# Kernel optimization log

Measured on AMD Instinct MI355X. Metric: run time of the kernel, lower is better.

Reference implementation:

```python
import jax, jax.numpy as jnp
import numpy as np

N_P, N_D, N_S = 100000, 1000, 5000      # patients, drugs, diseases
C, H, L = 64, 4, 2                       # hidden, heads, layers
DH = C // H                              # head dim
IN_P, IN_D, IN_S = 64, 128, 64           # raw feature dims per node type
E_PD, E_DP, E_DS, E_PS = 300000, 300000, 100000, 100000
EPS = 1e-16


def setup_inputs() -> dict:
    key = jax.random.key(0)
    ks = jax.random.split(key, 20)

    def lin(k, fin, fout, prefix=()):
        return jax.random.normal(k, prefix + (fin, fout), jnp.float32) / np.sqrt(fin).astype(np.float32)

    def edges(k, e, n_src, n_dst):
        k1, k2 = jax.random.split(k)
        return jnp.stack([jax.random.randint(k1, (e,), 0, n_src),
                          jax.random.randint(k2, (e,), 0, n_dst)]).astype(jnp.int32)

    inp = {}
    inp['x_p'] = jax.random.normal(ks[0], (N_P, IN_P), jnp.float32)
    inp['x_d'] = jax.random.normal(ks[1], (N_D, IN_D), jnp.float32)
    inp['x_s'] = jax.random.normal(ks[2], (N_S, IN_S), jnp.float32)
    inp['Win_p'] = lin(ks[3], IN_P, C); inp['bin_p'] = jnp.zeros((C,), jnp.float32)
    inp['Win_d'] = lin(ks[4], IN_D, C); inp['bin_d'] = jnp.zeros((C,), jnp.float32)
    inp['Win_s'] = lin(ks[5], IN_S, C); inp['bin_s'] = jnp.zeros((C,), jnp.float32)
    inp['Wk'] = lin(ks[6], C, C, (L, 3)); inp['bk'] = jnp.zeros((L, 3, C), jnp.float32)
    inp['Wq'] = lin(ks[7], C, C, (L, 3)); inp['bq'] = jnp.zeros((L, 3, C), jnp.float32)
    inp['Wv'] = lin(ks[8], C, C, (L, 3)); inp['bv'] = jnp.zeros((L, 3, C), jnp.float32)
    inp['Wa'] = lin(ks[9], C, C, (L, 3)); inp['ba'] = jnp.zeros((L, 3, C), jnp.float32)
    inp['a_rel'] = jax.random.normal(ks[10], (L, 4, H, DH, DH), jnp.float32) / np.sqrt(DH).astype(np.float32)
    inp['m_rel'] = jax.random.normal(ks[11], (L, 4, H, DH, DH), jnp.float32) / np.sqrt(DH).astype(np.float32)
    inp['p_rel'] = jnp.ones((L, 4, H), jnp.float32)   # PyG inits rel prior to ones
    inp['skip'] = jnp.ones((L, 3), jnp.float32)       # PyG inits skip gate to ones
    inp['ei_pd'] = edges(ks[12], E_PD, N_P, N_D)  # patient -takes-> drug
    inp['ei_dp'] = edges(ks[13], E_DP, N_D, N_P)  # drug -taken_by-> patient
    inp['ei_ds'] = edges(ks[14], E_DS, N_D, N_S)  # drug -treats-> disease
    inp['ei_ps'] = edges(ks[15], E_PS, N_P, N_S)  # patient -has-> disease
    return inp


def _hgt(x_p, x_d, x_s, Win_p, bin_p, Win_d, bin_d, Win_s, bin_s,
         Wk, bk, Wq, bq, Wv, bv, Wa, ba, a_rel, m_rel, p_rel, skip,
         ei_pd, ei_dp, ei_ds, ei_ps):
    Ns = (N_P, N_D, N_S)
    # per-node-type input projection (lin_dict)
    xs = [x_p @ Win_p + bin_p, x_d @ Win_d + bin_d, x_s @ Win_s + bin_s]
    # (src_type, dst_type, edge_index) for each relation
    edge_defs = [(0, 1, ei_pd), (1, 0, ei_dp), (1, 2, ei_ds), (0, 2, ei_ps)]
    inv_sqrt_d = np.float32(1.0 / np.sqrt(DH))

    for l in range(L):  # HGTConv layers
        k_t = [(xs[t] @ Wk[l, t] + bk[l, t]).reshape(Ns[t], H, DH) for t in range(3)]
        q_t = [(xs[t] @ Wq[l, t] + bq[l, t]).reshape(Ns[t], H, DH) for t in range(3)]
        v_t = [(xs[t] @ Wv[l, t] + bv[l, t]).reshape(Ns[t], H, DH) for t in range(3)]
        out = [jnp.zeros((Ns[t], H, DH), xs[t].dtype) for t in range(3)]
        for r, (st, dt, ei) in enumerate(edge_defs):
            src, dst = ei[0], ei[1]
            # relation-specific head-wise transforms of K and V
            k_rel = jnp.einsum('nhd,hde->nhe', k_t[st], a_rel[l, r])
            v_rel = jnp.einsum('nhd,hde->nhe', v_t[st], m_rel[l, r])
            # attention logits per edge, per head: [E, H]
            alpha = (q_t[dt][dst] * k_rel[src]).sum(-1) * (p_rel[l, r] * inv_sqrt_d)
            # segment softmax over incoming edges of each dst node (per relation)
            mx = jax.ops.segment_max(alpha, dst, num_segments=Ns[dt])
            a = jnp.exp(alpha - jax.lax.stop_gradient(mx)[dst])
            den = jax.ops.segment_sum(a, dst, num_segments=Ns[dt])
            a = a / (den[dst] + EPS)
            # attention-weighted scatter-add of messages, grouped by 'sum'
            out[dt] = out[dt] + jax.ops.segment_sum(v_rel[src] * a[:, :, None], dst, num_segments=Ns[dt])
        new_xs = []
        for t in range(3):
            o = jax.nn.gelu(out[t].reshape(Ns[t], C), approximate=False) @ Wa[l, t] + ba[l, t]
            s = jax.nn.sigmoid(skip[l, t])  # learned skip gate (in == out channels)
            new_xs.append(s * o + (1.0 - s) * xs[t])
        xs = new_xs
    # concatenate node-type outputs along node axis: [N_P+N_D+N_S, C]
    return jnp.concatenate(xs, axis=0)


def reference(x_p, x_d, x_s, Win_p, bin_p, Win_d, bin_d, Win_s, bin_s,
              Wk, bk, Wq, bq, Wv, bv, Wa, ba, a_rel, m_rel, p_rel, skip,
              ei_pd, ei_dp, ei_ds, ei_ps):
    return _hgt(x_p, x_d, x_s, Win_p, bin_p, Win_d, bin_d, Win_s, bin_s,
                Wk, bk, Wq, bq, Wv, bv, Wa, ba, a_rel, m_rel, p_rel, skip,
                ei_pd, ei_dp, ei_ds, ei_ps)
```

## Files before the change

kernel.cpp:

```cpp
#include <hip/hip_runtime.h>
#include <cmath>

typedef unsigned short ush;
typedef __attribute__((ext_vector_type(8))) short short8;
typedef __attribute__((ext_vector_type(4))) float floatx4;

static constexpr int N_P = 100000, N_D = 1000, N_S = 5000, NT = N_P + N_D + N_S;
static constexpr int NC = 111000;
static constexpr int E_TOT = 800000;

static constexpr int NB0 = 128, NB2 = 64, NB3 = 64;
static constexpr int CH0 = (300000 + NB0 - 1) / NB0;
static constexpr int CH2 = (100000 + NB2 - 1) / NB2;
static constexpr int HB0_OFF = 0;
static constexpr int HB2_OFF = NB0 * 1000;
static constexpr int HB3_OFF = HB2_OFF + NB2 * 5000;
static constexpr int NCH0 = NB0 / 16, NCH2 = NB2 / 16;
static constexpr int CS0_OFF = 0;
static constexpr int CS2_OFF = NCH0 * 1000;
static constexpr int CS3_OFF = CS2_OFF + NCH2 * 5000;
static constexpr int NHIST = NB0 + NB2 + NB3;
static constexpr int NBLK_R1 = (300000 + 255) / 256;

__device__ __forceinline__ float b2f(ush b) { return __uint_as_float(((unsigned)b) << 16); }
__device__ __forceinline__ ush f2b(float f) {
    unsigned u = __float_as_uint(f);
    return (ush)((u + 0x7FFFu + ((u >> 16) & 1u)) >> 16);
}

__global__ __launch_bounds__(256) void detect_kernel(const ush* __restrict__ xp,
                                                     int* __restrict__ flag) {
    __shared__ int s;
    if (threadIdx.x == 0) s = 0;
    __syncthreads();
    int c = 0;
    for (int i = threadIdx.x; i < 16384; i += 256) {
        ush h = xp[i];
        if ((h & 0x7F80) == 0x7F80) c = 1;
    }
    if (c) atomicOr(&s, 1);
    __syncthreads();
    if (threadIdx.x == 0) *flag = s;
}

struct ConvArgs {
    const void* src[21];
    long cum[22];
};

__global__ __launch_bounds__(256) void convert_kernel(ConvArgs a, ush* __restrict__ dst,
                                                      long total, const int* __restrict__ flag) {
    const int f = *flag;
    for (long g = (long)blockIdx.x * 256 + threadIdx.x; g < total; g += (long)gridDim.x * 256) {
        int t = 0;
        while (g >= a.cum[t + 1]) t++;
        long i = g - a.cum[t];
        float v = f ? ((const float*)a.src[t])[i] : b2f(((const ush*)a.src[t])[i]);
        dst[g] = f2b(v);
    }
}

static constexpr size_t OFF_XP = 0;
static constexpr size_t OFF_XD = 6400000;
static constexpr size_t OFF_XS = 6528000;
static constexpr size_t OFF_WINP = 6848000;
static constexpr size_t OFF_BINP = 6852096;
static constexpr size_t OFF_WIND = 6852160;
static constexpr size_t OFF_BIND = 6860352;
static constexpr size_t OFF_WINS = 6860416;
static constexpr size_t OFF_BINS = 6864512;
static constexpr size_t OFF_WK = 6864576;
static constexpr size_t OFF_BK = 6889152;
static constexpr size_t OFF_WQ = 6889536;
static constexpr size_t OFF_BQ = 6914112;
static constexpr size_t OFF_WV = 6914496;
static constexpr size_t OFF_BV = 6939072;
static constexpr size_t OFF_WA = 6939456;
static constexpr size_t OFF_BA = 6964032;
static constexpr size_t OFF_AREL = 6964416;
static constexpr size_t OFF_MREL = 6972608;
static constexpr size_t OFF_PREL = 6980800;
static constexpr size_t OFF_SKIP = 6980832;
static constexpr size_t CW_TOTAL = 6980838;

struct CsrB {
    const int* ei[3];
    const int* ei1;
};

__device__ __forceinline__ void hist_geom(int b, const CsrB& c, int& r, const int*& ei, int& E,
                                          int& ndst, int& e0, int& e1, int& hb) {
    if (b < NB0) {
        r = 0; ei = c.ei[0]; E = 300000; ndst = 1000;
        e0 = b * CH0; hb = HB0_OFF + b * 1000;
    } else if (b < NB0 + NB2) {
        r = 1; ei = c.ei[1]; E = 100000; ndst = 5000;
        e0 = (b - NB0) * CH2; hb = HB2_OFF + (b - NB0) * 5000;
    } else {
        r = 2; ei = c.ei[2]; E = 100000; ndst = 5000;
        e0 = (b - NB0 - NB2) * CH2; hb = HB3_OFF + (b - NB0 - NB2) * 5000;
    }
    e1 = min(E, e0 + ((r == 0) ? CH0 : CH2));
}

__global__ __launch_bounds__(256) void count_kernel(CsrB c, int* __restrict__ HB,
                                                    int* __restrict__ cnt) {
    const int b = blockIdx.x;
    if (b >= NHIST) {
        int g = (b - NHIST) * 256 + threadIdx.x;
        if (g < 300000) atomicAdd(&cnt[1000 + c.ei1[300000 + g]], 1);
        return;
    }
    __shared__ int h[5000];
    int r, E, ndst, e0, e1, hb;
    const int* ei;
    hist_geom(b, c, r, ei, E, ndst, e0, e1, hb);
    for (int d = threadIdx.x; d < ndst; d += 256) h[d] = 0;
    __syncthreads();
    for (int e = e0 + threadIdx.x; e < e1; e += 256) atomicAdd(&h[ei[E + e]], 1);
    __syncthreads();
    for (int d = threadIdx.x; d < ndst; d += 256) HB[hb + d] = h[d];
}

__device__ __forceinline__ bool cs_geom(int g, int& idx0, int& step) {
    if (g >= 48000) return false;
    if (g < 8000) {
        int c = g / 1000, d = g % 1000;
        idx0 = HB0_OFF + c * 16 * 1000 + d; step = 1000;
    } else if (g < 28000) {
        int gg = g - 8000, c = gg / 5000, d = gg % 5000;
        idx0 = HB2_OFF + c * 16 * 5000 + d; step = 5000;
    } else {
        int gg = g - 28000, c = gg / 5000, d = gg % 5000;
        idx0 = HB3_OFF + c * 16 * 5000 + d; step = 5000;
    }
    return true;
}

__global__ __launch_bounds__(256) void sumHB_kernel(const int* __restrict__ HB,
                                                    int* __restrict__ CS) {
    int g = blockIdx.x * 256 + threadIdx.x;
    int idx0, step;
    if (!cs_geom(g, idx0, step)) return;
    int s = 0;
#pragma unroll
    for (int b = 0; b < 16; b++) s += HB[idx0 + b * step];
    CS[g] = s;
}

__global__ __launch_bounds__(256) void scanCS_kernel(int* __restrict__ CS,
                                                     int* __restrict__ cnt) {
    int d = blockIdx.x * 256 + threadIdx.x;
    if (d >= 11000) return;
    int ld, nch, cs0, step, roff;
    if (d < 1000) { ld = d; nch = NCH0; cs0 = CS0_OFF + ld; step = 1000; roff = 0; }
    else if (d < 6000) { ld = d - 1000; nch = NCH2; cs0 = CS2_OFF + ld; step = 5000; roff = 101000; }
    else { ld = d - 6000; nch = NCH2; cs0 = CS3_OFF + ld; step = 5000; roff = 106000; }
    int run = 0;
    for (int c = 0; c < nch; c++) {
        int t = CS[cs0 + c * step];
        CS[cs0 + c * step] = run;
        run += t;
    }
    cnt[roff + ld] = run;
}

__global__ __launch_bounds__(256) void fixHB_kernel(int* __restrict__ HB,
                                                    const int* __restrict__ CS) {
    int g = blockIdx.x * 256 + threadIdx.x;
    int idx0, step;
    if (!cs_geom(g, idx0, step)) return;
    int run = CS[g];
#pragma unroll
    for (int b = 0; b < 16; b++) {
        int t = HB[idx0 + b * step];
        HB[idx0 + b * step] = run;
        run += t;
    }
}

__global__ __launch_bounds__(256) void scanA_kernel(const int* __restrict__ cnt,
                                                    int* __restrict__ tmp,
                                                    int* __restrict__ part) {
    __shared__ int ls[256];
    const int t = threadIdx.x;
    const int base = blockIdx.x * 1024 + t * 4;
    int v[4];
#pragma unroll
    for (int j = 0; j < 4; j++) v[j] = (base + j < NC) ? cnt[base + j] : 0;
    int tsum = v[0] + v[1] + v[2] + v[3];
    ls[t] = tsum;
    __syncthreads();
    for (int off = 1; off < 256; off <<= 1) {
        int y = (t >= off) ? ls[t - off] : 0;
        __syncthreads();
        ls[t] += y;
        __syncthreads();
    }
    int run = ls[t] - tsum;
#pragma unroll
    for (int j = 0; j < 4; j++) {
        if (base + j < NC) tmp[base + j] = run;
        run += v[j];
    }
    if (t == 255) part[blockIdx.x] = ls[255];
}

__global__ __launch_bounds__(256) void scanB_kernel(int* __restrict__ part, int nb) {
    __shared__ int ls[256];
    const int t = threadIdx.x;
    int x = (t < nb) ? part[t] : 0;
    ls[t] = x;
    __syncthreads();
    for (int off = 1; off < 256; off <<= 1) {
        int y = (t >= off) ? ls[t - off] : 0;
        __syncthreads();
        ls[t] += y;
        __syncthreads();
    }
    if (t < nb) part[t] = ls[t] - x;
    if (t == nb - 1) part[nb] = ls[t];
}

__global__ __launch_bounds__(256) void scanC_kernel(const int* __restrict__ tmp,
                                                    const int* __restrict__ part,
                                                    int* __restrict__ rowptr) {
    int i = blockIdx.x * 256 + threadIdx.x;
    if (i > NC) return;
    rowptr[i] = (i == NC) ? part[(NC + 1023) / 1024] : tmp[i] + part[i >> 10];
}

__global__ __launch_bounds__(256) void fill_kernel(CsrB c, const int* __restrict__ HB,
                                                   const int* __restrict__ rowptr,
                                                   int* __restrict__ fillpos,
                                                   int* __restrict__ col) {
    const int b = blockIdx.x;
    if (b >= NHIST) {
        int g = (b - NHIST) * 256 + threadIdx.x;
        if (g < 300000) {
            int gi = 1000 + c.ei1[300000 + g];
            int slot = rowptr[gi] + atomicAdd(&fillpos[gi], 1);
            col[slot] = c.ei1[g];
        }
        return;
    }
    __shared__ int h[5000];
    int r, E, ndst, e0, e1, hb;
    const int* ei;
    hist_geom(b, c, r, ei, E, ndst, e0, e1, hb);
    const int roff = (r == 0) ? 0 : (r == 1) ? 101000 : 106000;
    for (int d = threadIdx.x; d < ndst; d += 256) h[d] = rowptr[roff + d] + HB[hb + d];
    __syncthreads();
    for (int e = e0 + threadIdx.x; e < e1; e += 256) {
        int d = ei[E + e];
        int slot = atomicAdd(&h[d], 1);
        col[slot] = ei[e];
    }
}

__global__ __launch_bounds__(256) void eff_kernel(const ush* __restrict__ CW,
                                                  ush* __restrict__ weff) {
    const int b = blockIdx.x;
    const int l = b >> 2, r = b & 3;
    const int st_of[4] = {0, 1, 1, 0};
    const int st = st_of[r];
    ush* out = weff + (size_t)b * 8320;
    for (int idx = threadIdx.x; idx < 8320; idx += 256) {
        int n, k;
        if (idx < 8192) { k = idx >> 7; n = idx & 127; }
        else { k = -1; n = idx - 8192; }
        int kv = n >= 64;
        int j = n & 63, h = j >> 4, e = j & 15;
        const ush* W = CW + (kv ? OFF_WV : OFF_WK) + (size_t)(l * 3 + st) * 4096;
        const ush* B = CW + (kv ? OFF_BV : OFF_BK) + (size_t)(l * 3 + st) * 64;
        const ush* R = CW + (kv ? OFF_MREL : OFF_AREL) + (size_t)(l * 4 + r) * 1024;
        float acc = 0.f;
        if (k >= 0) {
#pragma unroll
            for (int d = 0; d < 16; d++)
                acc += b2f(W[k * 64 + h * 16 + d]) * b2f(R[h * 256 + d * 16 + e]);
        } else {
#pragma unroll
            for (int d = 0; d < 16; d++)
                acc += b2f(B[h * 16 + d]) * b2f(R[h * 256 + d * 16 + e]);
        }
        out[idx] = f2b(acc);
    }
}

template <int K, int NOUT>
__device__ __forceinline__ void gemm_tile(const ush* __restrict__ X, const ush* __restrict__ W,
                                          const ush* __restrict__ Bb, ush* __restrict__ Y,
                                          int M, int row0) {
    constexpr int NF = (K / 32) * (NOUT / 16);
    __shared__ short sA[64][K + 8];
    __shared__ short sB[NF][512];
    const int tid = threadIdx.x;
    for (int cid = tid; cid < 64 * K / 8; cid += 256) {
        int r = cid / (K / 8), c0 = (cid % (K / 8)) * 8;
        int row = row0 + r;
        short8 v = {0, 0, 0, 0, 0, 0, 0, 0};
        if (row < M) v = *(const short8*)(const void*)(X + (size_t)row * K + c0);
        *(short8*)(&sA[r][c0]) = v;
    }
    for (int u = tid; u < NF * 64; u += 256) {
        int f = u >> 6, l = u & 63;
        int s = f / (NOUT / 16), c = f % (NOUT / 16);
        int kbase = 32 * s + ((l >> 4) << 3), n = 16 * c + (l & 15);
        short8 v;
#pragma unroll
        for (int j = 0; j < 8; j++) v[j] = (short)W[(size_t)(kbase + j) * NOUT + n];
        *(short8*)(&sB[f][l * 8]) = v;
    }
    __syncthreads();
    const int w = tid >> 6, l = tid & 63;
    floatx4 acc[NOUT / 16];
#pragma unroll
    for (int c = 0; c < NOUT / 16; c++) {
        float bv = b2f(Bb[16 * c + (l & 15)]);
        acc[c] = (floatx4){bv, bv, bv, bv};
    }
#pragma unroll
    for (int s = 0; s < K / 32; s++) {
        short8 a = *(const short8*)(&sA[16 * w + (l & 15)][32 * s + ((l >> 4) << 3)]);
#pragma unroll
        for (int c = 0; c < NOUT / 16; c++) {
            short8 b = *(const short8*)(&sB[s * (NOUT / 16) + c][l * 8]);
            acc[c] = __builtin_amdgcn_mfma_f32_16x16x32_bf16(a, b, acc[c], 0, 0, 0);
        }
    }
#pragma unroll
    for (int c = 0; c < NOUT / 16; c++)
#pragma unroll
        for (int r = 0; r < 4; r++) {
            int row = row0 + 16 * w + ((l >> 4) << 2) + r;
            if (row < M) Y[(size_t)row * NOUT + 16 * c + (l & 15)] = f2b(acc[c][r]);
        }
}

template <int K, int NOUT>
__global__ __launch_bounds__(256) void mfma_proj(const ush* __restrict__ X,
                                                 const ush* __restrict__ W,
                                                 const ush* __restrict__ bias,
                                                 ush* __restrict__ Y, int M) {
    gemm_tile<K, NOUT>(X, W, bias, Y, M, blockIdx.x * 64);
}

struct QArgs {
    const ush* X;
    ush* Q;
    const ush* W[3];
    const ush* Bb[3];
};
__global__ __launch_bounds__(256) void qproj_kernel(QArgs a) {
    const int b = blockIdx.x;
    int t, lb, M;
    size_t noff;
    if (b < 1563) { t = 0; lb = b; M = N_P; noff = 0; }
    else if (b < 1579) { t = 1; lb = b - 1563; M = N_D; noff = (size_t)N_P; }
    else { t = 2; lb = b - 1579; M = N_S; noff = (size_t)(N_P + N_D); }
    gemm_tile<64, 64>(a.X + noff * 64, a.W[t], a.Bb[t], a.Q + noff * 64, M, lb * 64);
}

struct KVArgs {
    const ush* X[4];
    ush* Y[4];
    const ush* W[4];
    const ush* Bb[4];
};
__global__ __launch_bounds__(256) void kvproj_kernel(KVArgs a) {
    const int b = blockIdx.x;
    int r, lb, M;
    if (b < 1563) { r = 0; lb = b; M = N_P; }
    else if (b < 1579) { r = 1; lb = b - 1563; M = N_D; }
    else if (b < 1595) { r = 2; lb = b - 1579; M = N_D; }
    else { r = 3; lb = b - 1595; M = N_P; }
    gemm_tile<64, 128>(a.X[r], a.W[r], a.Bb[r], a.Y[r], M, lb * 64);
}

struct AggrArgs {
    const int* rowptr;
    const int* col;
    const ush* KV[4];
    const ush* Q;
    const ush* prel;
    float* OUT;
};

template <int LANES>
__device__ __forceinline__ void seg_attn(const AggrArgs& a, int rel, int g, int h, int lane,
                                         const float* qf, float* o) {
    const int s0 = a.rowptr[g], s1 = a.rowptr[g + 1];
    const ush* KV = a.KV[rel];
    const float ps = b2f(a.prel[rel * 4 + h]) * 0.25f;
    float m = -1e30f, s = 0.f;
    float acc[16];
#pragma unroll
    for (int i = 0; i < 16; i++) acc[i] = 0.f;
    for (int j = s0 + lane; j < s1; j += LANES) {
        int src = a.col[j];
        const ush* kp = KV + (size_t)src * 128 + h * 16;
        short8 k0 = *(const short8*)(const void*)kp;
        short8 k1 = *(const short8*)(const void*)(kp + 8);
        short8 v0 = *(const short8*)(const void*)(kp + 64);
        short8 v1 = *(const short8*)(const void*)(kp + 72);
        float dot = 0.f;
#pragma unroll
        for (int i = 0; i < 8; i++) dot += qf[i] * b2f((ush)k0[i]);
#pragma unroll
        for (int i = 0; i < 8; i++) dot += qf[8 + i] * b2f((ush)k1[i]);
        float aa = dot * ps;
        float nm = fmaxf(m, aa);
        float e0 = __expf(m - nm), e1 = __expf(aa - nm);
        s = s * e0 + e1;
#pragma unroll
        for (int i = 0; i < 8; i++) acc[i] = acc[i] * e0 + e1 * b2f((ush)v0[i]);
#pragma unroll
        for (int i = 0; i < 8; i++) acc[8 + i] = acc[8 + i] * e0 + e1 * b2f((ush)v1[i]);
        m = nm;
    }
#pragma unroll
    for (int wd = LANES >> 1; wd >= 1; wd >>= 1) {
        float mo = __shfl_xor(m, wd);
        float so = __shfl_xor(s, wd);
        float nm = fmaxf(m, mo);
        float e0 = __expf(m - nm), e1 = __expf(mo - nm);
        s = s * e0 + so * e1;
#pragma unroll
        for (int i = 0; i < 16; i++) {
            float ao = __shfl_xor(acc[i], wd);
            acc[i] = acc[i] * e0 + ao * e1;
        }
        m = nm;
    }
    float inv = 1.f / (s + 1e-16f);
#pragma unroll
    for (int i = 0; i < 16; i++) o[i] += acc[i] * inv;
}

template <int LANES>
__device__ __forceinline__ void job_run(const AggrArgs& a, int wid, int nd, int rel, int roff,
                                        size_t xoff, int rel2, int roff2) {
    const int lane = wid % LANES;
    const int grp = wid / LANES;
    const int d = grp >> 2, h = grp & 3;
    if (d >= nd) return;
    const ush* qp = a.Q + xoff + (size_t)d * 64 + h * 16;
    short8 q0 = *(const short8*)(const void*)qp;
    short8 q1 = *(const short8*)(const void*)(qp + 8);
    float qf[16];
#pragma unroll
    for (int i = 0; i < 8; i++) { qf[i] = b2f((ush)q0[i]); qf[8 + i] = b2f((ush)q1[i]); }
    float o[16];
#pragma unroll
    for (int i = 0; i < 16; i++) o[i] = 0.f;
    seg_attn<LANES>(a, rel, roff + d, h, lane, qf, o);
    if (rel2 >= 0) seg_attn<LANES>(a, rel2, roff2 + d, h, lane, qf, o);
    if (lane == 0) {
        float* op = a.OUT + xoff + (size_t)d * 64 + h * 16;
#pragma unroll
        for (int i = 0; i < 4; i++)
            *(floatx4*)(op + 4 * i) =
                (floatx4){o[4 * i], o[4 * i + 1], o[4 * i + 2], o[4 * i + 3]};
    }
}

__global__ __launch_bounds__(256) void aggr_kernel(AggrArgs a) {
    const int b = blockIdx.x, t = threadIdx.x;
    if (b < 250) {
        job_run<16>(a, b * 256 + t, N_D, 0, 0, (size_t)N_P * 64, -1, 0);
    } else if (b < 563) {
        job_run<4>(a, (b - 250) * 256 + t, N_S, 2, 101000, (size_t)(N_P + N_D) * 64, 3, 106000);
    } else {
        job_run<2>(a, (b - 563) * 256 + t, N_P, 1, 1000, 0, -1, 0);
    }
}

struct EpiArgs {
    const float* O;
    ush* X;
    const ush* W[3];
    const ush* Bb[3];
    const ush* skipv;
    void* fout;
    const int* flag;
    int last;
};

__global__ __launch_bounds__(256) void epi_kernel(EpiArgs a) {
    const int b = blockIdx.x;
    int t, lb, M;
    size_t noff;
    if (b < 1563) { t = 0; lb = b; M = N_P; noff = 0; }
    else if (b < 1579) { t = 1; lb = b - 1563; M = N_D; noff = (size_t)N_P; }
    else { t = 2; lb = b - 1579; M = N_S; noff = (size_t)(N_P + N_D); }
    const float* O = a.O + noff * 64;
    ush* X = a.X + noff * 64;
    const ush* W = a.W[t];
    __shared__ short sA[64][72];
    __shared__ short sB[8][512];
    const int tid = threadIdx.x;
    const int row0 = lb * 64;
    for (int cid = tid; cid < 512; cid += 256) {
        int r = cid >> 3, c0 = (cid & 7) * 8;
        int row = row0 + r;
        short8 sv = {0, 0, 0, 0, 0, 0, 0, 0};
        if (row < M) {
#pragma unroll
            for (int j = 0; j < 8; j++) {
                float v = O[(size_t)row * 64 + c0 + j];
                sv[j] = (short)f2b(0.5f * v * (1.0f + erff(v * 0.70710678118654752f)));
            }
        }
        *(short8*)(&sA[r][c0]) = sv;
    }
    for (int u = tid; u < 512; u += 256) {
        int f = u >> 6, l = u & 63;
        int s = f >> 2, c = f & 3;
        int kbase = 32 * s + ((l >> 4) << 3), n = 16 * c + (l & 15);
        short8 v;
#pragma unroll
        for (int j = 0; j < 8; j++) v[j] = (short)W[(size_t)(kbase + j) * 64 + n];
        *(short8*)(&sB[f][l * 8]) = v;
    }
    __syncthreads();
    const int w = tid >> 6, l = tid & 63;
    const float sg = 1.f / (1.f + expf(-b2f(a.skipv[t])));
    floatx4 acc[4];
#pragma unroll
    for (int c = 0; c < 4; c++) {
        float bv = b2f(a.Bb[t][16 * c + (l & 15)]);
        acc[c] = (floatx4){bv, bv, bv, bv};
    }
#pragma unroll
    for (int s = 0; s < 2; s++) {
        short8 av = *(const short8*)(&sA[16 * w + (l & 15)][32 * s + ((l >> 4) << 3)]);
#pragma unroll
        for (int c = 0; c < 4; c++) {
            short8 bv = *(const short8*)(&sB[s * 4 + c][l * 8]);
            acc[c] = __builtin_amdgcn_mfma_f32_16x16x32_bf16(av, bv, acc[c], 0, 0, 0);
        }
    }
    const int fl = a.last ? *a.flag : 0;
#pragma unroll
    for (int c = 0; c < 4; c++)
#pragma unroll
        for (int r = 0; r < 4; r++) {
            int row = row0 + 16 * w + ((l >> 4) << 2) + r;
            if (row >= M) continue;
            size_t off = (size_t)row * 64 + 16 * c + (l & 15);
            float val = sg * acc[c][r] + (1.f - sg) * b2f(X[off]);
            if (!a.last) {
                X[off] = f2b(val);
            } else {
                size_t goff = (noff + row) * 64 + 16 * c + (l & 15);
                if (fl)
                    ((float*)a.fout)[goff] = val;
                else
                    ((ush*)a.fout)[goff] = f2b(val);
            }
        }
}

extern "C" void kernel_launch(void* const* d_in, const int* in_sizes, int n_in,
                              void* d_out, int out_size, void* d_ws, size_t ws_size,
                              hipStream_t stream) {
    char* w = (char*)d_ws;
    int* FLAG = (int*)w;    w += 64;
    ush* CW = (ush*)w;      w += ((CW_TOTAL * 2 + 63) / 64) * 64;
    ush* WEFFB = (ush*)w;   w += ((size_t)8 * 8320 * 2 + 63) / 64 * 64;
    ush* X = (ush*)w;       w += (size_t)NT * 64 * 2;
    ush* Q = (ush*)w;       w += (size_t)NT * 64 * 2;
    ush* KV0 = (ush*)w;     w += (size_t)N_P * 128 * 2;
    ush* KV1 = (ush*)w;     w += (size_t)N_D * 128 * 2;
    ush* KV2 = (ush*)w;     w += (size_t)N_D * 128 * 2;
    ush* KV3 = (ush*)w;     w += (size_t)N_P * 128 * 2;
    float* OUT = (float*)w; w += (size_t)NT * 64 * 4;
    int* CNT = (int*)w;     w += (size_t)NC * 4;
    int* TMP = (int*)w;     w += (size_t)NC * 4;
    int* PART = (int*)w;    w += 512;
    int* ROWPTR = (int*)w;  w += (size_t)(NC + 1) * 4;
    int* COL = (int*)w;     w += (size_t)E_TOT * 4;
    int* HB = (int*)OUT;
    int* CS = (int*)OUT + 800000;

    detect_kernel<<<1, 256, 0, stream>>>((const ush*)d_in[0], FLAG);
    static const long sz[21] = {6400000, 128000, 320000, 4096, 64, 8192, 64, 4096, 64,
                                24576, 384, 24576, 384, 24576, 384, 24576, 384,
                                8192, 8192, 32, 6};
    ConvArgs ca;
    long cum = 0;
    for (int t = 0; t < 21; t++) {
        ca.src[t] = d_in[t];
        ca.cum[t] = cum;
        cum += sz[t];
    }
    ca.cum[21] = cum;
    convert_kernel<<<4096, 256, 0, stream>>>(ca, CW, cum, FLAG);

    CsrB cb;
    cb.ei[0] = (const int*)d_in[21];
    cb.ei[1] = (const int*)d_in[23];
    cb.ei[2] = (const int*)d_in[24];
    cb.ei1 = (const int*)d_in[22];
    hipMemsetAsync(CNT + 1000, 0, (size_t)100000 * 4, stream);
    count_kernel<<<NHIST + NBLK_R1, 256, 0, stream>>>(cb, HB, CNT);
    sumHB_kernel<<<(48000 + 255) / 256, 256, 0, stream>>>(HB, CS);
    scanCS_kernel<<<(11000 + 255) / 256, 256, 0, stream>>>(CS, CNT);
    scanA_kernel<<<(NC + 1023) / 1024, 256, 0, stream>>>(CNT, TMP, PART);
    scanB_kernel<<<1, 256, 0, stream>>>(PART, (NC + 1023) / 1024);
    scanC_kernel<<<(NC + 1 + 255) / 256, 256, 0, stream>>>(TMP, PART, ROWPTR);
    hipMemsetAsync(CNT + 1000, 0, (size_t)100000 * 4, stream);
    fixHB_kernel<<<(48000 + 255) / 256, 256, 0, stream>>>(HB, CS);
    fill_kernel<<<NHIST + NBLK_R1, 256, 0, stream>>>(cb, HB, ROWPTR, CNT, COL);

    eff_kernel<<<8, 256, 0, stream>>>(CW, WEFFB);

    const size_t toff[3] = {0, (size_t)N_P, (size_t)(N_P + N_D)};

    mfma_proj<64, 64><<<(N_P + 63) / 64, 256, 0, stream>>>(
        CW + OFF_XP, CW + OFF_WINP, CW + OFF_BINP, X, N_P);
    mfma_proj<128, 64><<<(N_D + 63) / 64, 256, 0, stream>>>(
        CW + OFF_XD, CW + OFF_WIND, CW + OFF_BIND, X + toff[1] * 64, N_D);
    mfma_proj<64, 64><<<(N_S + 63) / 64, 256, 0, stream>>>(
        CW + OFF_XS, CW + OFF_WINS, CW + OFF_BINS, X + toff[2] * 64, N_S);

    for (int l = 0; l < 2; l++) {
        QArgs qa;
        qa.X = X;
        qa.Q = Q;
        for (int t = 0; t < 3; t++) {
            qa.W[t] = CW + OFF_WQ + (size_t)(l * 3 + t) * 4096;
            qa.Bb[t] = CW + OFF_BQ + (l * 3 + t) * 64;
        }
        qproj_kernel<<<1658, 256, 0, stream>>>(qa);

        KVArgs ka;
        ush* KVr[4] = {KV0, KV1, KV2, KV3};
        const int rst[4] = {0, 1, 1, 0};
        for (int r = 0; r < 4; r++) {
            ka.X[r] = X + toff[rst[r]] * 64;
            ka.Y[r] = KVr[r];
            const ush* we = WEFFB + (size_t)(l * 4 + r) * 8320;
            ka.W[r] = we;
            ka.Bb[r] = we + 8192;
        }
        kvproj_kernel<<<3158, 256, 0, stream>>>(ka);

        AggrArgs aa;
        aa.rowptr = ROWPTR;
        aa.col = COL;
        for (int r = 0; r < 4; r++) aa.KV[r] = KVr[r];
        aa.Q = Q;
        aa.prel = CW + OFF_PREL + l * 16;
        aa.OUT = OUT;
        aggr_kernel<<<3688, 256, 0, stream>>>(aa);

        EpiArgs ea;
        ea.O = OUT;
        ea.X = X;
        for (int t = 0; t < 3; t++) {
            ea.W[t] = CW + OFF_WA + (size_t)(l * 3 + t) * 4096;
            ea.Bb[t] = CW + OFF_BA + (l * 3 + t) * 64;
        }
        ea.skipv = CW + OFF_SKIP + l * 3;
        ea.fout = d_out;
        ea.flag = FLAG;
        ea.last = (l == 1) ? 1 : 0;
        epi_kernel<<<1658, 256, 0, stream>>>(ea);
    }
}
```

Measured before the change: 426.7 us.

## Fuse input conversion into projection, merge Q/KV kernels, fold memsets into kernels

The separate conversion of large node-feature tensors to bf16 is removed. The input projection now reads raw features directly (fp32 or bf16, chosen by a flag) and converts them while staging into shared memory, and the three input projections become one launch. The Q and KV projection kernels are merged into a single launch with dynamic shared memory, and the two memsets are folded into extra blocks of existing kernels. This saves a large round trip through memory and several launches, at the cost of more branching per block and a larger shared-memory footprint for the fused kernels.

```diff
diff --git a/kernel.cpp b/kernel.cpp
--- a/kernel.cpp
+++ b/kernel.cpp
@@ -21,6 +21,7 @@
 static constexpr int CS3_OFF = CS2_OFF + NCH2 * 5000;
 static constexpr int NHIST = NB0 + NB2 + NB3;
 static constexpr int NBLK_R1 = (300000 + 255) / 256;
+static constexpr int NZB = (100000 + 255) / 256;
 
 __device__ __forceinline__ float b2f(ush b) { return __uint_as_float(((unsigned)b) << 16); }
 __device__ __forceinline__ ush f2b(float f) {
@@ -43,45 +44,50 @@
     if (threadIdx.x == 0) *flag = s;
 }
 
+static constexpr size_t OFF_WINP = 0;
+static constexpr size_t OFF_BINP = 4096;
+static constexpr size_t OFF_WIND = 4160;
+static constexpr size_t OFF_BIND = 12352;
+static constexpr size_t OFF_WINS = 12416;
+static constexpr size_t OFF_BINS = 16512;
+static constexpr size_t OFF_WK = 16576;
+static constexpr size_t OFF_BK = 41152;
+static constexpr size_t OFF_WQ = 41536;
+static constexpr size_t OFF_BQ = 66112;
+static constexpr size_t OFF_WV = 66496;
+static constexpr size_t OFF_BV = 91072;
+static constexpr size_t OFF_WA = 91456;
+static constexpr size_t OFF_BA = 116032;
+static constexpr size_t OFF_AREL = 116416;
+static constexpr size_t OFF_MREL = 124608;
+static constexpr size_t OFF_PREL = 132800;
+static constexpr size_t OFF_SKIP = 132832;
+static constexpr size_t CW_TOTAL = 132838;
+static constexpr int NCONVB = (int)((CW_TOTAL + 255) / 256);
+
 struct ConvArgs {
-    const void* src[21];
-    long cum[22];
+    const void* src[18];
+    long cum[19];
 };
 
 __global__ __launch_bounds__(256) void convert_kernel(ConvArgs a, ush* __restrict__ dst,
-                                                      long total, const int* __restrict__ flag) {
+                                                      int* __restrict__ cnt_r1,
+                                                      const int* __restrict__ flag) {
+    const int b = blockIdx.x;
+    if (b >= NCONVB) {
+        int g = (b - NCONVB) * 256 + threadIdx.x;
+        if (g < 100000) cnt_r1[g] = 0;
+        return;
+    }
     const int f = *flag;
-    for (long g = (long)blockIdx.x * 256 + threadIdx.x; g < total; g += (long)gridDim.x * 256) {
-        int t = 0;
-        while (g >= a.cum[t + 1]) t++;
-        long i = g - a.cum[t];
-        float v = f ? ((const float*)a.src[t])[i] : b2f(((const ush*)a.src[t])[i]);
-        dst[g] = f2b(v);
-    }
-}
-
-static constexpr size_t OFF_XP = 0;
-static constexpr size_t OFF_XD = 6400000;
-static constexpr size_t OFF_XS = 6528000;
-static constexpr size_t OFF_WINP = 6848000;
-static constexpr size_t OFF_BINP = 6852096;
-static constexpr size_t OFF_WIND = 6852160;
-static constexpr size_t OFF_BIND = 6860352;
-static constexpr size_t OFF_WINS = 6860416;
-static constexpr size_t OFF_BINS = 6864512;
-static constexpr size_t OFF_WK = 6864576;
-static constexpr size_t OFF_BK = 6889152;
-static constexpr size_t OFF_WQ = 6889536;
-static constexpr size_t OFF_BQ = 6914112;
-static constexpr size_t OFF_WV = 6914496;
-static constexpr size_t OFF_BV = 6939072;
-static constexpr size_t OFF_WA = 6939456;
-static constexpr size_t OFF_BA = 6964032;
-static constexpr size_t OFF_AREL = 6964416;
-static constexpr size_t OFF_MREL = 6972608;
-static constexpr size_t OFF_PREL = 6980800;
-static constexpr size_t OFF_SKIP = 6980832;
-static constexpr size_t CW_TOTAL = 6980838;
+    long g = (long)b * 256 + threadIdx.x;
+    if (g >= (long)CW_TOTAL) return;
+    int t = 0;
+    while (g >= a.cum[t + 1]) t++;
+    long i = g - a.cum[t];
+    float v = f ? ((const float*)a.src[t])[i] : b2f(((const ush*)a.src[t])[i]);
+    dst[g] = f2b(v);
+}
 
 struct CsrB {
     const int* ei[3];
@@ -222,10 +228,18 @@
     if (t == nb - 1) part[nb] = ls[t];
 }
 
+static constexpr int NSCB = (NC + 1 + 255) / 256;
 __global__ __launch_bounds__(256) void scanC_kernel(const int* __restrict__ tmp,
                                                     const int* __restrict__ part,
-                                                    int* __restrict__ rowptr) {
-    int i = blockIdx.x * 256 + threadIdx.x;
+                                                    int* __restrict__ rowptr,
+                                                    int* __restrict__ cnt_r1) {
+    const int b = blockIdx.x;
+    if (b >= NSCB) {
+        int g = (b - NSCB) * 256 + threadIdx.x;
+        if (g < 100000) cnt_r1[g] = 0;
+        return;
+    }
+    int i = b * 256 + threadIdx.x;
     if (i > NC) return;
     rowptr[i] = (i == NC) ? part[(NC + 1023) / 1024] : tmp[i] + part[i >> 10];
 }
@@ -288,21 +302,46 @@
     }
 }
 
-template <int K, int NOUT>
-__device__ __forceinline__ void gemm_tile(const ush* __restrict__ X, const ush* __restrict__ W,
-                                          const ush* __restrict__ Bb, ush* __restrict__ Y,
-                                          int M, int row0) {
-    constexpr int NF = (K / 32) * (NOUT / 16);
-    __shared__ short sA[64][K + 8];
-    __shared__ short sB[NF][512];
-    const int tid = threadIdx.x;
-    for (int cid = tid; cid < 64 * K / 8; cid += 256) {
+template <int K>
+__device__ __forceinline__ void stage_A(short* sA, const ush* __restrict__ X, int M, int row0) {
+    for (int cid = threadIdx.x; cid < 64 * K / 8; cid += 256) {
         int r = cid / (K / 8), c0 = (cid % (K / 8)) * 8;
         int row = row0 + r;
         short8 v = {0, 0, 0, 0, 0, 0, 0, 0};
         if (row < M) v = *(const short8*)(const void*)(X + (size_t)row * K + c0);
-        *(short8*)(&sA[r][c0]) = v;
-    }
+        *(short8*)(&sA[r * (K + 8) + c0]) = v;
+    }
+}
+
+template <int K>
+__device__ __forceinline__ void stage_A_raw(short* sA, const void* __restrict__ X, int f,
+                                            int M, int row0) {
+    for (int cid = threadIdx.x; cid < 64 * K / 8; cid += 256) {
+        int r = cid / (K / 8), c0 = (cid % (K / 8)) * 8;
+        int row = row0 + r;
+        short8 v = {0, 0, 0, 0, 0, 0, 0, 0};
+        if (row < M) {
+            if (f) {
+                const floatx4* fp = (const floatx4*)((const float*)X + (size_t)row * K + c0);
+                floatx4 f0 = fp[0], f1 = fp[1];
+#pragma unroll
+                for (int j = 0; j < 4; j++) v[j] = (short)f2b(f0[j]);
+#pragma unroll
+                for (int j = 0; j < 4; j++) v[4 + j] = (short)f2b(f1[j]);
+            } else {
+                v = *(const short8*)(const void*)((const ush*)X + (size_t)row * K + c0);
+            }
+        }
+        *(short8*)(&sA[r * (K + 8) + c0]) = v;
+    }
+}
+
+template <int K, int NOUT>
+__device__ __forceinline__ void gemm_core(const short* sA, short* sB,
+                                          const ush* __restrict__ W, const ush* __restrict__ Bb,
+                                          ush* __restrict__ Y, int M, int row0) {
+    constexpr int NF = (K / 32) * (NOUT / 16);
+    const int tid = threadIdx.x;
     for (int u = tid; u < NF * 64; u += 256) {
         int f = u >> 6, l = u & 63;
         int s = f / (NOUT / 16), c = f % (NOUT / 16);
@@ -310,7 +349,7 @@
         short8 v;
 #pragma unroll
         for (int j = 0; j < 8; j++) v[j] = (short)W[(size_t)(kbase + j) * NOUT + n];
-        *(short8*)(&sB[f][l * 8]) = v;
+        *(short8*)(&sB[f * 512 + l * 8]) = v;
     }
     __syncthreads();
     const int w = tid >> 6, l = tid & 63;
@@ -322,10 +361,10 @@
     }
 #pragma unroll
     for (int s = 0; s < K / 32; s++) {
-        short8 a = *(const short8*)(&sA[16 * w + (l & 15)][32 * s + ((l >> 4) << 3)]);
+        short8 a = *(const short8*)(&sA[(16 * w + (l & 15)) * (K + 8) + 32 * s + ((l >> 4) << 3)]);
 #pragma unroll
         for (int c = 0; c < NOUT / 16; c++) {
-            short8 b = *(const short8*)(&sB[s * (NOUT / 16) + c][l * 8]);
+            short8 b = *(const short8*)(&sB[(s * (NOUT / 16) + c) * 512 + l * 8]);
             acc[c] = __builtin_amdgcn_mfma_f32_16x16x32_bf16(a, b, acc[c], 0, 0, 0);
         }
     }
@@ -338,44 +377,72 @@
         }
 }
 
-template <int K, int NOUT>
-__global__ __launch_bounds__(256) void mfma_proj(const ush* __restrict__ X,
-                                                 const ush* __restrict__ W,
-                                                 const ush* __restrict__ bias,
-                                                 ush* __restrict__ Y, int M) {
-    gemm_tile<K, NOUT>(X, W, bias, Y, M, blockIdx.x * 64);
-}
-
-struct QArgs {
+struct InArgs {
+    const void* raw[3];
+    const ush* W[3];
+    const ush* Bb[3];
+    ush* X;
+    const int* flag;
+};
+
+__global__ __launch_bounds__(256) void inproj_kernel(InArgs a) {
+    extern __shared__ short smem[];
+    const int b = blockIdx.x;
+    const int f = *a.flag;
+    if (b < 1563) {
+        short* sA = smem;
+        short* sB = smem + 64 * 72;
+        stage_A_raw<64>(sA, a.raw[0], f, N_P, b * 64);
+        gemm_core<64, 64>(sA, sB, a.W[0], a.Bb[0], a.X, N_P, b * 64);
+    } else if (b < 1579) {
+        short* sA = smem;
+        short* sB = smem + 64 * 136;
+        stage_A_raw<128>(sA, a.raw[1], f, N_D, (b - 1563) * 64);
+        gemm_core<128, 64>(sA, sB, a.W[1], a.Bb[1], a.X + (size_t)N_P * 64, N_D,
+                           (b - 1563) * 64);
+    } else {
+        short* sA = smem;
+        short* sB = smem + 64 * 72;
+        stage_A_raw<64>(sA, a.raw[2], f, N_S, (b - 1579) * 64);
+        gemm_core<64, 64>(sA, sB, a.W[2], a.Bb[2], a.X + (size_t)(N_P + N_D) * 64, N_S,
+                          (b - 1579) * 64);
+    }
+}
+
+struct QKVArgs {
     const ush* X;
     ush* Q;
-    const ush* W[3];
-    const ush* Bb[3];
+    const ush* Wq[3];
+    const ush* Bq[3];
+    const ush* Xr[4];
+    ush* Y[4];
+    const ush* Wkv[4];
+    const ush* Bkv[4];
 };
-__global__ __launch_bounds__(256) void qproj_kernel(QArgs a) {
+
+__global__ __launch_bounds__(256) void qkv_kernel(QKVArgs a) {
+    extern __shared__ short smem[];
+    short* sA = smem;
+    short* sB = smem + 64 * 72;
     const int b = blockIdx.x;
-    int t, lb, M;
-    size_t noff;
-    if (b < 1563) { t = 0; lb = b; M = N_P; noff = 0; }
-    else if (b < 1579) { t = 1; lb = b - 1563; M = N_D; noff = (size_t)N_P; }
-    else { t = 2; lb = b - 1579; M = N_S; noff = (size_t)(N_P + N_D); }
-    gemm_tile<64, 64>(a.X + noff * 64, a.W[t], a.Bb[t], a.Q + noff * 64, M, lb * 64);
-}
-
-struct KVArgs {
-    const ush* X[4];
-    ush* Y[4];
-    const ush* W[4];
-    const ush* Bb[4];
-};
-__global__ __launch_bounds__(256) void kvproj_kernel(KVArgs a) {
-    const int b = blockIdx.x;
-    int r, lb, M;
-    if (b < 1563) { r = 0; lb = b; M = N_P; }
-    else if (b < 1579) { r = 1; lb = b - 1563; M = N_D; }
-    else if (b < 1595) { r = 2; lb = b - 1579; M = N_D; }
-    else { r = 3; lb = b - 1595; M = N_P; }
-    gemm_tile<64, 128>(a.X[r], a.W[r], a.Bb[r], a.Y[r], M, lb * 64);
+    if (b < 1658) {
+        int t, lb, M;
+        size_t noff;
+        if (b < 1563) { t = 0; lb = b; M = N_P; noff = 0; }
+        else if (b < 1579) { t = 1; lb = b - 1563; M = N_D; noff = (size_t)N_P; }
+        else { t = 2; lb = b - 1579; M = N_S; noff = (size_t)(N_P + N_D); }
+        stage_A<64>(sA, a.X + noff * 64, M, lb * 64);
+        gemm_core<64, 64>(sA, sB, a.Wq[t], a.Bq[t], a.Q + noff * 64, M, lb * 64);
+    } else {
+        int bb = b - 1658;
+        int r, lb, M;
+        if (bb < 1563) { r = 0; lb = bb; M = N_P; }
+        else if (bb < 1579) { r = 1; lb = bb - 1563; M = N_D; }
+        else if (bb < 1595) { r = 2; lb = bb - 1579; M = N_D; }
+        else { r = 3; lb = bb - 1595; M = N_P; }
+        stage_A<64>(sA, a.Xr[r], M, lb * 64);
+        gemm_core<64, 128>(sA, sB, a.Wkv[r], a.Bkv[r], a.Y[r], M, lb * 64);
+    }
 }
 
 struct AggrArgs {
@@ -497,8 +564,8 @@
     const float* O = a.O + noff * 64;
     ush* X = a.X + noff * 64;
     const ush* W = a.W[t];
-    __shared__ short sA[64][72];
-    __shared__ short sB[8][512];
+    __shared__ short sA[64 * 72];
+    __shared__ short sB[8 * 512];
     const int tid = threadIdx.x;
     const int row0 = lb * 64;
     for (int cid = tid; cid < 512; cid += 256) {
@@ -512,8 +579,10 @@
                 sv[j] = (short)f2b(0.5f * v * (1.0f + erff(v * 0.70710678118654752f)));
             }
         }
-        *(short8*)(&sA[r][c0]) = sv;
-    }
+        *(short8*)(&sA[r * 72 + c0]) = sv;
+    }
+    __syncthreads();
+    const float sg = 1.f / (1.f + expf(-b2f(a.skipv[t])));
     for (int u = tid; u < 512; u += 256) {
         int f = u >> 6, l = u & 63;
         int s = f >> 2, c = f & 3;
@@ -521,11 +590,10 @@
         short8 v;
 #pragma unroll
         for (int j = 0; j < 8; j++) v[j] = (short)W[(size_t)(kbase + j) * 64 + n];
-        *(short8*)(&sB[f][l * 8]) = v;
+        *(short8*)(&sB[f * 512 + l * 8]) = v;
     }
     __syncthreads();
     const int w = tid >> 6, l = tid & 63;
-    const float sg = 1.f / (1.f + expf(-b2f(a.skipv[t])));
     floatx4 acc[4];
 #pragma unroll
     for (int c = 0; c < 4; c++) {
@@ -534,10 +602,10 @@
     }
 #pragma unroll
     for (int s = 0; s < 2; s++) {
-        short8 av = *(const short8*)(&sA[16 * w + (l & 15)][32 * s + ((l >> 4) << 3)]);
+        short8 av = *(const short8*)(&sA[(16 * w + (l & 15)) * 72 + 32 * s + ((l >> 4) << 3)]);
 #pragma unroll
         for (int c = 0; c < 4; c++) {
-            short8 bv = *(const short8*)(&sB[s * 4 + c][l * 8]);
+            short8 bv = *(const short8*)(&sB[(s * 4 + c) * 512 + l * 8]);
             acc[c] = __builtin_amdgcn_mfma_f32_16x16x32_bf16(av, bv, acc[c], 0, 0, 0);
         }
     }
@@ -585,32 +653,29 @@
     int* CS = (int*)OUT + 800000;
 
     detect_kernel<<<1, 256, 0, stream>>>((const ush*)d_in[0], FLAG);
-    static const long sz[21] = {6400000, 128000, 320000, 4096, 64, 8192, 64, 4096, 64,
-                                24576, 384, 24576, 384, 24576, 384, 24576, 384,
-                                8192, 8192, 32, 6};
+    static const long sz[18] = {4096, 64, 8192, 64, 4096, 64, 24576, 384, 24576, 384,
+                                24576, 384, 24576, 384, 8192, 8192, 32, 6};
     ConvArgs ca;
     long cum = 0;
-    for (int t = 0; t < 21; t++) {
-        ca.src[t] = d_in[t];
+    for (int t = 0; t < 18; t++) {
+        ca.src[t] = d_in[3 + t];
         ca.cum[t] = cum;
         cum += sz[t];
     }
-    ca.cum[21] = cum;
-    convert_kernel<<<4096, 256, 0, stream>>>(ca, CW, cum, FLAG);
+    ca.cum[18] = cum;
+    convert_kernel<<<NCONVB + NZB, 256, 0, stream>>>(ca, CW, CNT + 1000, FLAG);
 
     CsrB cb;
     cb.ei[0] = (const int*)d_in[21];
     cb.ei[1] = (const int*)d_in[23];
     cb.ei[2] = (const int*)d_in[24];
     cb.ei1 = (const int*)d_in[22];
-    hipMemsetAsync(CNT + 1000, 0, (size_t)100000 * 4, stream);
     count_kernel<<<NHIST + NBLK_R1, 256, 0, stream>>>(cb, HB, CNT);
     sumHB_kernel<<<(48000 + 255) / 256, 256, 0, stream>>>(HB, CS);
     scanCS_kernel<<<(11000 + 255) / 256, 256, 0, stream>>>(CS, CNT);
     scanA_kernel<<<(NC + 1023) / 1024, 256, 0, stream>>>(CNT, TMP, PART);
     scanB_kernel<<<1, 256, 0, stream>>>(PART, (NC + 1023) / 1024);
-    scanC_kernel<<<(NC + 1 + 255) / 256, 256, 0, stream>>>(TMP, PART, ROWPTR);
-    hipMemsetAsync(CNT + 1000, 0, (size_t)100000 * 4, stream);
+    scanC_kernel<<<NSCB + NZB, 256, 0, stream>>>(TMP, PART, ROWPTR, CNT + 1000);
     fixHB_kernel<<<(48000 + 255) / 256, 256, 0, stream>>>(HB, CS);
     fill_kernel<<<NHIST + NBLK_R1, 256, 0, stream>>>(cb, HB, ROWPTR, CNT, COL);
 
@@ -618,34 +683,35 @@
 
     const size_t toff[3] = {0, (size_t)N_P, (size_t)(N_P + N_D)};
 
-    mfma_proj<64, 64><<<(N_P + 63) / 64, 256, 0, stream>>>(
-        CW + OFF_XP, CW + OFF_WINP, CW + OFF_BINP, X, N_P);
-    mfma_proj<128, 64><<<(N_D + 63) / 64, 256, 0, stream>>>(
-        CW + OFF_XD, CW + OFF_WIND, CW + OFF_BIND, X + toff[1] * 64, N_D);
-    mfma_proj<64, 64><<<(N_S + 63) / 64, 256, 0, stream>>>(
-        CW + OFF_XS, CW + OFF_WINS, CW + OFF_BINS, X + toff[2] * 64, N_S);
+    InArgs ia;
+    ia.raw[0] = d_in[0];
+    ia.raw[1] = d_in[1];
+    ia.raw[2] = d_in[2];
+    ia.W[0] = CW + OFF_WINP; ia.Bb[0] = CW + OFF_BINP;
+    ia.W[1] = CW + OFF_WIND; ia.Bb[1] = CW + OFF_BIND;
+    ia.W[2] = CW + OFF_WINS; ia.Bb[2] = CW + OFF_BINS;
+    ia.X = X;
+    ia.flag = FLAG;
+    inproj_kernel<<<1658, 256, 33792, stream>>>(ia);
 
     for (int l = 0; l < 2; l++) {
-        QArgs qa;
-        qa.X = X;
-        qa.Q = Q;
-        for (int t = 0; t < 3; t++) {
-            qa.W[t] = CW + OFF_WQ + (size_t)(l * 3 + t) * 4096;
-            qa.Bb[t] = CW + OFF_BQ + (l * 3 + t) * 64;
-        }
-        qproj_kernel<<<1658, 256, 0, stream>>>(qa);
-
-        KVArgs ka;
+        QKVArgs qk;
+        qk.X = X;
+        qk.Q = Q;
         ush* KVr[4] = {KV0, KV1, KV2, KV3};
         const int rst[4] = {0, 1, 1, 0};
+        for (int t = 0; t < 3; t++) {
+            qk.Wq[t] = CW + OFF_WQ + (size_t)(l * 3 + t) * 4096;
+            qk.Bq[t] = CW + OFF_BQ + (l * 3 + t) * 64;
+        }
         for (int r = 0; r < 4; r++) {
-            ka.X[r] = X + toff[rst[r]] * 64;
-            ka.Y[r] = KVr[r];
+            qk.Xr[r] = X + toff[rst[r]] * 64;
+            qk.Y[r] = KVr[r];
             const ush* we = WEFFB + (size_t)(l * 4 + r) * 8320;
-            ka.W[r] = we;
-            ka.Bb[r] = we + 8192;
-        }
-        kvproj_kernel<<<3158, 256, 0, stream>>>(ka);
+            qk.Wkv[r] = we;
+            qk.Bkv[r] = we + 8192;
+        }
+        qkv_kernel<<<4816, 256, 25600, stream>>>(qk);
 
         AggrArgs aa;
         aa.rowptr = ROWPTR;
```

New measurement: 396.6 us. -7.1%, faster.
